# Optimization experiments

Measured on AMD Instinct MI355X. Metric: run time of the kernel, lower is better.

## Reference

```python
import jax, jax.numpy as jnp
import numpy as np

H, W = 64, 64
B, P, F = 8, 512, 512
EXPAND = 0.02      # bbox expansion for soft silhouette (NDC units), DIB-R default
MULT = 1000.0      # DIB-R coordinate multiplier
DELTA = 7000.0     # soft prob falloff in multiplier-scaled squared units, DIB-R default
EPS = 1e-10


def setup_inputs() -> dict:
    key = jax.random.key(0)
    k1, k2, k3 = jax.random.split(key, 3)
    verts = 0.5 * jax.random.normal(k1, (B, P, 3), dtype=jnp.float32)
    faces = jax.random.randint(k2, (B, F, 3), 0, P, dtype=jnp.int32)
    colors = jax.random.uniform(k3, (B, P, 3), dtype=jnp.float32)
    camera_rot = jnp.tile(jnp.eye(3, dtype=jnp.float32)[None], (B, 1, 1))
    camera_pos = jnp.tile(jnp.array([0.0, 0.0, 3.0], dtype=jnp.float32)[None], (B, 1))
    fov_factor = 2.7475  # 1 / tan(fovy/2), fovy ~ 0.7 rad, aspect 1
    camera_proj = jnp.array([[fov_factor], [fov_factor], [-1.0]], dtype=jnp.float32)
    return {"verts": verts, "faces": faces, "camera_rot": camera_rot,
            "camera_pos": camera_pos, "camera_proj": camera_proj, "colors": colors}


def _render_one(verts_p3, faces_f3, rot_33, pos_3, proj_31, colors_p3):
    # --- perspective_projection (pixel2mesh convention: p' = rot^T (p - pos)) ---
    pcam = (verts_p3 - pos_3[None, :]) @ rot_33.T                 # [P,3] camera frame
    xy3 = pcam * proj_31.reshape(3)[None, :]
    xy = xy3[:, :2] / xy3[:, 2:3]                                  # [P,2] NDC
    tri3d = pcam[faces_f3]                                         # [F,3,3]
    tri2d = xy[faces_f3]                                           # [F,3,2]
    normal = jnp.cross(tri3d[:, 1] - tri3d[:, 0], tri3d[:, 2] - tri3d[:, 0])  # [F,3]
    normalz = normal[:, 2]
    normal1 = normal / (jnp.linalg.norm(normal, axis=1, keepdims=True) + 1e-12)
    # per-face vertex colors + hard-mask channel -> [F,3,4] (== color_1xfx12)
    cmask = jnp.ones((faces_f3.shape[0], 3, 1), dtype=colors_p3.dtype)
    cfeat = jnp.concatenate([colors_p3[faces_f3], cmask], axis=2)

    # --- linear_rasterizer: pixel grid in NDC ---
    xs = (2.0 * jnp.arange(W, dtype=jnp.float32) + 1.0 - W) / W
    ys = (H - 2.0 * jnp.arange(H, dtype=jnp.float32) - 1.0) / H
    x0 = xs[None, :, None]                                         # [1,W,1]
    y0 = ys[:, None, None]                                         # [H,1,1]
    ax, ay = tri2d[:, 0, 0], tri2d[:, 0, 1]
    bx, by = tri2d[:, 1, 0], tri2d[:, 1, 1]
    cx, cy = tri2d[:, 2, 0], tri2d[:, 2, 1]
    det = (by - cy) * (ax - cx) + (cx - bx) * (ay - cy)            # [F]
    det_safe = jnp.where(jnp.abs(det) < EPS, EPS, det)
    w0 = ((by - cy) * (x0 - cx) + (cx - bx) * (y0 - cy)) / det_safe  # [H,W,F]
    w1 = ((cy - ay) * (x0 - cx) + (ax - cx) * (y0 - cy)) / det_safe
    w2 = 1.0 - w0 - w1
    z = w0 * tri3d[:, 0, 2] + w1 * tri3d[:, 1, 2] + w2 * tri3d[:, 2, 2]  # [H,W,F]
    covered = (w0 >= 0) & (w1 >= 0) & (w2 >= 0)
    valid = covered & (normalz > 0) & (jnp.abs(det) > EPS)
    # hard z-buffer: camera looks along -z, so nearest face has max z
    zbuf = jnp.where(valid, z, -1e10)
    best = jnp.argmax(zbuf, axis=-1)                               # [H,W]
    anyv = jnp.any(valid, axis=-1)
    gw = lambda w: jnp.take_along_axis(w, best[..., None], axis=-1)[..., 0]
    g0, g1, g2 = gw(w0), gw(w1), gw(w2)
    cb = cfeat[best]                                               # [H,W,3,4]
    feat = (g0[..., None] * cb[..., 0, :] + g1[..., None] * cb[..., 1, :]
            + g2[..., None] * cb[..., 2, :])
    imfeat = jnp.where(anyv[..., None], feat, 0.0)                 # [H,W,4]

    # --- soft silhouette probability ---
    def seg_d2(px, py, qx, qy):
        vx, vy = qx - px, qy - py
        t = jnp.clip(((x0 - px) * vx + (y0 - py) * vy)
                     / (vx * vx + vy * vy + 1e-12), 0.0, 1.0)
        dx, dy = x0 - (px + t * vx), y0 - (py + t * vy)
        return dx * dx + dy * dy
    d2 = jnp.minimum(jnp.minimum(seg_d2(ax, ay, bx, by), seg_d2(bx, by, cx, cy)),
                     seg_d2(cx, cy, ax, ay))
    d2 = jnp.where(covered, 0.0, d2)                               # inside -> 0
    xmin = jnp.minimum(jnp.minimum(ax, bx), cx) - EXPAND
    xmax = jnp.maximum(jnp.maximum(ax, bx), cx) + EXPAND
    ymin = jnp.minimum(jnp.minimum(ay, by), cy) - EXPAND
    ymax = jnp.maximum(jnp.maximum(ay, by), cy) + EXPAND
    in_bbox = (x0 >= xmin) & (x0 <= xmax) & (y0 >= ymin) & (y0 <= ymax)
    contrib = jnp.where(in_bbox, jnp.exp(-d2 * (MULT * MULT) / DELTA), 0.0)
    improb = 1.0 - jnp.prod(1.0 - contrib, axis=-1, keepdims=True)  # [H,W,1]
    return imfeat, improb, normal1


def reference(verts, faces, camera_rot, camera_pos, camera_proj, colors):
    imfeat, improb, normal1 = jax.vmap(_render_one, in_axes=(0, 0, 0, 0, None, 0))(
        verts, faces, camera_rot, camera_pos, camera_proj, colors)
    imrender = imfeat[..., :3]     # [B,H,W,3]
    hardmask = imfeat[..., 3:]     # [B,H,W,1]
    return imrender, improb, normal1, hardmask
```

## Files before the change

kernel.cpp:

```cpp
#include <hip/hip_runtime.h>
#include <math.h>

#define NB 8
#define NP 512
#define NF 512
#define NH 64
#define NW 64
#define FEXPAND 0.02f
#define FEPS 1e-10f

#define IMG_OFF 0
#define PROB_OFF (NB*NH*NW*3)
#define NRM_OFF  (PROB_OFF + NB*NH*NW)
#define MASK_OFF (NRM_OFF + NB*NF*3)

__global__ __launch_bounds__(1024, 8) void render_all(
    const float* __restrict__ verts, const int* __restrict__ faces,
    const float* __restrict__ rot, const float* __restrict__ pos,
    const float* __restrict__ proj, const float* __restrict__ colors,
    float* __restrict__ out)
{
  __shared__ __align__(16) float smem[NF*28];
  __shared__ unsigned short flist[NF];
  __shared__ int wcnt[8];
  __shared__ int Ltot;
  int tid  = threadIdx.x;
  int b    = blockIdx.x >> 6;
  int tile = blockIdx.x & 63;
  int wave = tid >> 6;
  int lane = tid & 63;
  int ix0 = (tile & 7)*8, iy0 = (tile >> 3)*8;
  int ix = ix0 + (lane & 7);
  int iy = iy0 + (lane >> 3);
  float x = (2.0f*ix + 1.0f - 64.0f) * (1.0f/64.0f);
  float y = (64.0f - 2.0f*iy - 1.0f) * (1.0f/64.0f);
  float txlo = (2.0f*ix0 + 1.0f - 64.0f) * (1.0f/64.0f);
  float txhi = (2.0f*(ix0+7) + 1.0f - 64.0f) * (1.0f/64.0f);
  float tyhi = (64.0f - 2.0f*iy0 - 1.0f) * (1.0f/64.0f);
  float tylo = (64.0f - 2.0f*(iy0+7) - 1.0f) * (1.0f/64.0f);

  if (tid < NF) {
    int t = b * NF + tid;
    float p0 = proj[0], p1 = proj[1], p2 = proj[2];
    float R0=rot[b*9+0],R1=rot[b*9+1],R2=rot[b*9+2];
    float R3=rot[b*9+3],R4=rot[b*9+4],R5=rot[b*9+5];
    float R6=rot[b*9+6],R7=rot[b*9+7],R8=rot[b*9+8];
    float ppx=pos[b*3+0], ppy=pos[b*3+1], ppz=pos[b*3+2];
    int idxs[3] = { faces[t*3+0], faces[t*3+1], faces[t*3+2] };
    float X[3],Y[3],Z[3],SX[3],SY[3];
#pragma unroll
    for (int k = 0; k < 3; ++k) {
      const float* v = verts + ((size_t)b*NP + idxs[k])*3;
      float dx = v[0]-ppx, dy = v[1]-ppy, dz = v[2]-ppz;
      float pcx = __fadd_rn(__fadd_rn(__fmul_rn(R0,dx),__fmul_rn(R1,dy)),__fmul_rn(R2,dz));
      float pcy = __fadd_rn(__fadd_rn(__fmul_rn(R3,dx),__fmul_rn(R4,dy)),__fmul_rn(R5,dz));
      float pcz = __fadd_rn(__fadd_rn(__fmul_rn(R6,dx),__fmul_rn(R7,dy)),__fmul_rn(R8,dz));
      X[k]=pcx; Y[k]=pcy; Z[k]=pcz;
      float dn = __fmul_rn(pcz, p2);
      SX[k] = __fdiv_rn(__fmul_rn(pcx, p0), dn);
      SY[k] = __fdiv_rn(__fmul_rn(pcy, p1), dn);
    }
    float e1x=X[1]-X[0], e1y=Y[1]-Y[0], e1z=Z[1]-Z[0];
    float e2x=X[2]-X[0], e2y=Y[2]-Y[0], e2z=Z[2]-Z[0];
    float nzel = __fsub_rn(__fmul_rn(e1x,e2y), __fmul_rn(e1y,e2x));
    if (tile == 0) {
      float m0 = __fmul_rn(e1z, e2y); float nxf = __fmaf_rn(e1y, e2z, -m0);
      float m1 = __fmul_rn(e1x, e2z); float nyf = __fmaf_rn(e1z, e2x, -m1);
      float m2 = __fmul_rn(e1y, e2x); float nzf = __fmaf_rn(e1x, e2y, -m2);
      float nn = __fsqrt_rn(__fadd_rn(__fadd_rn(__fmul_rn(nxf,nxf),__fmul_rn(nyf,nyf)),
                                      __fmul_rn(nzf,nzf)));
      float den = __fadd_rn(nn, 1e-12f);
      out[NRM_OFF + (size_t)t*3+0] = __fdiv_rn(nxf, den);
      out[NRM_OFF + (size_t)t*3+1] = __fdiv_rn(nyf, den);
      out[NRM_OFF + (size_t)t*3+2] = __fdiv_rn(nzf, den);
    }
    float ax=SX[0],ay=SY[0],bx=SX[1],by=SY[1],cx=SX[2],cy=SY[2];
    float det = __fadd_rn(__fmul_rn(__fsub_rn(by,cy),__fsub_rn(ax,cx)),
                          __fmul_rn(__fsub_rn(cx,bx),__fsub_rn(ay,cy)));
    float det_safe = (fabsf(det) < FEPS) ? FEPS : det;
    float validf = ((nzel > 0.0f) && (fabsf(det) > FEPS)) ? 1.0f : 0.0f;
    float* d = &smem[tid*28];
    d[0]=__fsub_rn(by,cy); d[1]=__fsub_rn(cx,bx);
    d[2]=__fsub_rn(cy,ay); d[3]=__fsub_rn(ax,cx);
    d[4]=cx; d[5]=cy; d[6]=det_safe; d[7]=validf;
    d[8]=Z[0]; d[9]=Z[1]; d[10]=Z[2];
    float vx=bx-ax, vy=by-ay;
    d[11]=1.0f/(vx*vx+vy*vy+1e-12f);
    d[20]=vx; d[21]=vy;
    d[12]=fminf(fminf(ax,bx),cx)-FEXPAND; d[13]=fmaxf(fmaxf(ax,bx),cx)+FEXPAND;
    d[14]=fminf(fminf(ay,by),cy)-FEXPAND; d[15]=fmaxf(fmaxf(ay,by),cy)+FEXPAND;
    d[16]=ax; d[17]=ay; d[18]=bx; d[19]=by;
    vx=cx-bx; vy=cy-by;
    d[22]=vx; d[23]=vy; d[26]=1.0f/(vx*vx+vy*vy+1e-12f);
    vx=ax-cx; vy=ay-cy;
    d[24]=vx; d[25]=vy; d[27]=1.0f/(vx*vx+vy*vy+1e-12f);
  }
  __syncthreads();

  bool pass = false;
  if (tid < NF) {
    const float* rr = &smem[tid*28 + 12];
    pass = (rr[1] >= txlo) && (rr[0] <= txhi) && (rr[3] >= tylo) && (rr[2] <= tyhi);
  }
  unsigned long long m = __ballot(pass);
  if (tid < NF && (tid & 63) == 0) wcnt[tid >> 6] = __popcll(m);
  __syncthreads();
  if (tid < NF && pass) {
    int w8 = tid >> 6;
    int off = 0;
#pragma unroll
    for (int i = 0; i < 8; ++i) if (i < w8) off += wcnt[i];
    off += __popcll(m & ((1ull << (tid & 63)) - 1ull));
    flist[off] = (unsigned short)tid;
  }
  if (tid == 0) {
    int s = 0;
#pragma unroll
    for (int i = 0; i < 8; ++i) s += wcnt[i];
    Ltot = s;
  }
  __syncthreads();
  int L = Ltot;

  float bestz = -1e10f;
  int   bestf = 0;
  float bw0 = 0.0f, bw1 = 0.0f, bw2 = 0.0f;
  float prod  = 1.0f;

  int idx = wave;
  int fcur = (idx < L) ? (int)flist[idx] : 0;
  float4 bb = (idx < L) ? *(const float4*)&smem[fcur*28 + 12]
                        : make_float4(0.f,0.f,0.f,0.f);
  while (idx < L) {
    int nidx = idx + 16;
    int fnext = fcur;
    float4 bbn = bb;
    if (nidx < L) {
      fnext = (int)flist[nidx];
      bbn = *(const float4*)&smem[fnext*28 + 12];
    }
    int f = fcur;
    const float* r = &smem[f*28];
    bool inb = (x >= bb.x) && (x <= bb.y) && (y >= bb.z) && (y <= bb.w);
    bool covered = false;
    if (__any(inb)) {
      float4 qe = *(const float4*)(r);
      float4 q1 = *(const float4*)(r + 4);
      float dxc = x - q1.x, dyc = y - q1.y;
      float n0 = __fadd_rn(__fmul_rn(qe.x, dxc), __fmul_rn(qe.y, dyc));
      float n1 = __fadd_rn(__fmul_rn(qe.z, dxc), __fmul_rn(qe.w, dyc));
      bool dsp  = q1.z > 0.0f;
      bool spass = ((n0 == 0.0f) || ((n0 > 0.0f) == dsp)) &&
                   ((n1 == 0.0f) || ((n1 > 0.0f) == dsp));
      bool act = inb && spass;
      if (__any(act)) {
        float4 q2 = *(const float4*)(r + 8);
        float w0 = __fdiv_rn(n0, q1.z);
        float w1 = __fdiv_rn(n1, q1.z);
        float w2 = __fsub_rn(__fsub_rn(1.0f, w0), w1);
        covered = act && (w2 >= 0.0f);
        bool valid = covered && (q1.w > 0.5f);
        float z = __fadd_rn(__fadd_rn(__fmul_rn(w0,q2.x), __fmul_rn(w1,q2.y)),
                            __fmul_rn(w2,q2.z));
        float zval = valid ? z : -1e10f;
        if (zval > bestz) { bestz = zval; bestf = f; bw0 = w0; bw1 = w1; bw2 = w2; }
      }
      if (covered) prod = 0.0f;
      bool needd = inb && !covered && (prod != 0.0f);
      if (__any(needd)) {
        float4 qa = *(const float4*)(r + 16);
        float4 qv = *(const float4*)(r + 20);
        float4 qw = *(const float4*)(r + 24);
        float invAB = r[11];
        float dxa = x - qa.x, dya = y - qa.y;
        float t1 = fminf(fmaxf((dxa*qv.x + dya*qv.y)*invAB, 0.0f), 1.0f);
        float rx = dxa - t1*qv.x, ry = dya - t1*qv.y;
        float d2 = rx*rx + ry*ry;
        float dxb = x - qa.z, dyb = y - qa.w;
        t1 = fminf(fmaxf((dxb*qv.z + dyb*qv.w)*qw.z, 0.0f), 1.0f);
        rx = dxb - t1*qv.z; ry = dyb - t1*qv.w;
        d2 = fminf(d2, rx*rx + ry*ry);
        t1 = fminf(fmaxf((dxc*qw.x + dyc*qw.y)*qw.w, 0.0f), 1.0f);
        rx = dxc - t1*qw.x; ry = dyc - t1*qw.y;
        d2 = fminf(d2, rx*rx + ry*ry);
        if (needd)
          prod *= (1.0f - __expf(d2 * -142.85714285714286f));
      }
    }
    idx = nidx; fcur = fnext; bb = bbn;
  }

  __syncthreads();
  float* comb = smem;
  float* c = comb + (size_t)(wave*64 + lane)*7;
  c[0]=bestz; c[1]=__int_as_float(bestf); c[2]=prod;
  c[3]=bw0; c[4]=bw1; c[5]=bw2;
  __syncthreads();

  if (tid < 64) {
    const float* c0 = comb + (size_t)tid*7;
    float bz = c0[0]; int bf = __float_as_int(c0[1]); float pr = c0[2];
    float w0 = c0[3], w1 = c0[4], w2 = c0[5];
    for (int s = 1; s < 16; ++s) {
      const float* cs = comb + (size_t)(s*64 + tid)*7;
      float oz = cs[0]; int of = __float_as_int(cs[1]);
      if (oz > bz || (oz == bz && of < bf)) { bz = oz; bf = of; w0 = cs[3]; w1 = cs[4]; w2 = cs[5]; }
      pr *= cs[2];
    }
    int av = (bz != -1e10f);
    int t = b * NF + bf;
    const int* fi = faces + (size_t)t*3;
    const float* cb = colors + (size_t)b*NP*3;
    int i0 = fi[0], i1 = fi[1], i2 = fi[2];
    float fr  = w0*cb[i0*3+0] + w1*cb[i1*3+0] + w2*cb[i2*3+0];
    float fgc = w0*cb[i0*3+1] + w1*cb[i1*3+1] + w2*cb[i2*3+1];
    float fb  = w0*cb[i0*3+2] + w1*cb[i1*3+2] + w2*cb[i2*3+2];
    float fa  = __fadd_rn(__fadd_rn(w0, w1), w2);
    int gp = b*4096 + iy*64 + ix;
    out[IMG_OFF + (size_t)gp*3 + 0] = av ? fr  : 0.0f;
    out[IMG_OFF + (size_t)gp*3 + 1] = av ? fgc : 0.0f;
    out[IMG_OFF + (size_t)gp*3 + 2] = av ? fb  : 0.0f;
    out[PROB_OFF + gp] = 1.0f - pr;
    out[MASK_OFF + gp] = av ? fa : 0.0f;
  }
}

extern "C" void kernel_launch(void* const* d_in, const int* in_sizes, int n_in,
                              void* d_out, int out_size, void* d_ws, size_t ws_size,
                              hipStream_t stream) {
  const float* verts  = (const float*)d_in[0];
  const int*   faces  = (const int*)  d_in[1];
  const float* rot    = (const float*)d_in[2];
  const float* pos    = (const float*)d_in[3];
  const float* proj   = (const float*)d_in[4];
  const float* colors = (const float*)d_in[5];
  float* out = (float*)d_out;
  (void)d_ws; (void)ws_size;

  hipLaunchKernelGGL(render_all, dim3(NB*64), dim3(1024), 0, stream,
                     verts, faces, rot, pos, proj, colors, out);
}
```

Baseline: 89.46 us.

## Split renderer into face setup, rasterize, and merge kernels via workspace

Before, every 1024-thread block recomputed all 512 face setups for its batch in shared memory. Now a separate kernel computes per-face records and normals once and writes them to the global workspace. The raster kernel reads those records from global memory, using 4 smaller 256-thread blocks per tile with each wave taking one face slice. A third kernel merges the 16 per-slice partial results. This removes redundant setup work and shared-memory pressure but adds two launches, global round trips of roughly 12.6 MB of partials, and global rather than LDS reads of the face records.

```diff
diff --git a/kernel.cpp b/kernel.cpp
--- a/kernel.cpp
+++ b/kernel.cpp
@@ -14,22 +14,87 @@
 #define NRM_OFF  (PROB_OFF + NB*NH*NW)
 #define MASK_OFF (NRM_OFF + NB*NF*3)
 
-__global__ __launch_bounds__(1024, 8) void render_all(
+#define REC0 4194304
+
+__global__ __launch_bounds__(256, 4) void face_setup(
     const float* __restrict__ verts, const int* __restrict__ faces,
     const float* __restrict__ rot, const float* __restrict__ pos,
-    const float* __restrict__ proj, const float* __restrict__ colors,
+    const float* __restrict__ proj, float* __restrict__ ws,
     float* __restrict__ out)
 {
-  __shared__ __align__(16) float smem[NF*28];
+  int t = blockIdx.x * 256 + threadIdx.x;
+  if (t >= NB * NF) return;
+  int b = t >> 9;
+  float p0 = proj[0], p1 = proj[1], p2 = proj[2];
+  float R0=rot[b*9+0],R1=rot[b*9+1],R2=rot[b*9+2];
+  float R3=rot[b*9+3],R4=rot[b*9+4],R5=rot[b*9+5];
+  float R6=rot[b*9+6],R7=rot[b*9+7],R8=rot[b*9+8];
+  float ppx=pos[b*3+0], ppy=pos[b*3+1], ppz=pos[b*3+2];
+  int idxs[3] = { faces[t*3+0], faces[t*3+1], faces[t*3+2] };
+  float X[3],Y[3],Z[3],SX[3],SY[3];
+#pragma unroll
+  for (int k = 0; k < 3; ++k) {
+    const float* v = verts + ((size_t)b*NP + idxs[k])*3;
+    float dx = v[0]-ppx, dy = v[1]-ppy, dz = v[2]-ppz;
+    float pcx = __fadd_rn(__fadd_rn(__fmul_rn(R0,dx),__fmul_rn(R1,dy)),__fmul_rn(R2,dz));
+    float pcy = __fadd_rn(__fadd_rn(__fmul_rn(R3,dx),__fmul_rn(R4,dy)),__fmul_rn(R5,dz));
+    float pcz = __fadd_rn(__fadd_rn(__fmul_rn(R6,dx),__fmul_rn(R7,dy)),__fmul_rn(R8,dz));
+    X[k]=pcx; Y[k]=pcy; Z[k]=pcz;
+    float dn = __fmul_rn(pcz, p2);
+    SX[k] = __fdiv_rn(__fmul_rn(pcx, p0), dn);
+    SY[k] = __fdiv_rn(__fmul_rn(pcy, p1), dn);
+  }
+  float e1x=X[1]-X[0], e1y=Y[1]-Y[0], e1z=Z[1]-Z[0];
+  float e2x=X[2]-X[0], e2y=Y[2]-Y[0], e2z=Z[2]-Z[0];
+  float nzel = __fsub_rn(__fmul_rn(e1x,e2y), __fmul_rn(e1y,e2x));
+  float m0 = __fmul_rn(e1z, e2y); float nxf = __fmaf_rn(e1y, e2z, -m0);
+  float m1 = __fmul_rn(e1x, e2z); float nyf = __fmaf_rn(e1z, e2x, -m1);
+  float m2 = __fmul_rn(e1y, e2x); float nzf = __fmaf_rn(e1x, e2y, -m2);
+  float nn = __fsqrt_rn(__fadd_rn(__fadd_rn(__fmul_rn(nxf,nxf),__fmul_rn(nyf,nyf)),
+                                  __fmul_rn(nzf,nzf)));
+  float den = __fadd_rn(nn, 1e-12f);
+  out[NRM_OFF + (size_t)t*3+0] = __fdiv_rn(nxf, den);
+  out[NRM_OFF + (size_t)t*3+1] = __fdiv_rn(nyf, den);
+  out[NRM_OFF + (size_t)t*3+2] = __fdiv_rn(nzf, den);
+
+  float ax=SX[0],ay=SY[0],bx=SX[1],by=SY[1],cx=SX[2],cy=SY[2];
+  float det = __fadd_rn(__fmul_rn(__fsub_rn(by,cy),__fsub_rn(ax,cx)),
+                        __fmul_rn(__fsub_rn(cx,bx),__fsub_rn(ay,cy)));
+  float det_safe = (fabsf(det) < FEPS) ? FEPS : det;
+  float validf = ((nzel > 0.0f) && (fabsf(det) > FEPS)) ? 1.0f : 0.0f;
+  float* d = ws + REC0 + (size_t)t*28;
+  d[0]=__fsub_rn(by,cy); d[1]=__fsub_rn(cx,bx);
+  d[2]=__fsub_rn(cy,ay); d[3]=__fsub_rn(ax,cx);
+  d[4]=cx; d[5]=cy; d[6]=det_safe; d[7]=validf;
+  d[8]=Z[0]; d[9]=Z[1]; d[10]=Z[2];
+  float vx=bx-ax, vy=by-ay;
+  d[11]=1.0f/(vx*vx+vy*vy+1e-12f);
+  d[20]=vx; d[21]=vy;
+  d[12]=fminf(fminf(ax,bx),cx)-FEXPAND; d[13]=fmaxf(fmaxf(ax,bx),cx)+FEXPAND;
+  d[14]=fminf(fminf(ay,by),cy)-FEXPAND; d[15]=fmaxf(fmaxf(ay,by),cy)+FEXPAND;
+  d[16]=ax; d[17]=ay; d[18]=bx; d[19]=by;
+  vx=cx-bx; vy=cy-by;
+  d[22]=vx; d[23]=vy; d[26]=1.0f/(vx*vx+vy*vy+1e-12f);
+  vx=ax-cx; vy=ay-cy;
+  d[24]=vx; d[25]=vy; d[27]=1.0f/(vx*vx+vy*vy+1e-12f);
+}
+
+__global__ __launch_bounds__(256, 4) void raster(
+    const float* __restrict__ ws_ro, float* __restrict__ ws,
+    const int* __restrict__ faces)
+{
   __shared__ unsigned short flist[NF];
   __shared__ int wcnt[8];
   __shared__ int Ltot;
   int tid  = threadIdx.x;
-  int b    = blockIdx.x >> 6;
-  int tile = blockIdx.x & 63;
+  int T    = blockIdx.x >> 2;
+  int sb   = blockIdx.x & 3;
   int wave = tid >> 6;
   int lane = tid & 63;
-  int ix0 = (tile & 7)*8, iy0 = (tile >> 3)*8;
+  int slice = sb*4 + wave;
+  int b    = T >> 6;
+  int txy  = T & 63;
+  int ix0 = (txy & 7)*8, iy0 = (txy >> 3)*8;
   int ix = ix0 + (lane & 7);
   int iy = iy0 + (lane >> 3);
   float x = (2.0f*ix + 1.0f - 64.0f) * (1.0f/64.0f);
@@ -38,80 +103,25 @@
   float txhi = (2.0f*(ix0+7) + 1.0f - 64.0f) * (1.0f/64.0f);
   float tyhi = (64.0f - 2.0f*iy0 - 1.0f) * (1.0f/64.0f);
   float tylo = (64.0f - 2.0f*(iy0+7) - 1.0f) * (1.0f/64.0f);
-
-  if (tid < NF) {
-    int t = b * NF + tid;
-    float p0 = proj[0], p1 = proj[1], p2 = proj[2];
-    float R0=rot[b*9+0],R1=rot[b*9+1],R2=rot[b*9+2];
-    float R3=rot[b*9+3],R4=rot[b*9+4],R5=rot[b*9+5];
-    float R6=rot[b*9+6],R7=rot[b*9+7],R8=rot[b*9+8];
-    float ppx=pos[b*3+0], ppy=pos[b*3+1], ppz=pos[b*3+2];
-    int idxs[3] = { faces[t*3+0], faces[t*3+1], faces[t*3+2] };
-    float X[3],Y[3],Z[3],SX[3],SY[3];
-#pragma unroll
-    for (int k = 0; k < 3; ++k) {
-      const float* v = verts + ((size_t)b*NP + idxs[k])*3;
-      float dx = v[0]-ppx, dy = v[1]-ppy, dz = v[2]-ppz;
-      float pcx = __fadd_rn(__fadd_rn(__fmul_rn(R0,dx),__fmul_rn(R1,dy)),__fmul_rn(R2,dz));
-      float pcy = __fadd_rn(__fadd_rn(__fmul_rn(R3,dx),__fmul_rn(R4,dy)),__fmul_rn(R5,dz));
-      float pcz = __fadd_rn(__fadd_rn(__fmul_rn(R6,dx),__fmul_rn(R7,dy)),__fmul_rn(R8,dz));
-      X[k]=pcx; Y[k]=pcy; Z[k]=pcz;
-      float dn = __fmul_rn(pcz, p2);
-      SX[k] = __fdiv_rn(__fmul_rn(pcx, p0), dn);
-      SY[k] = __fdiv_rn(__fmul_rn(pcy, p1), dn);
-    }
-    float e1x=X[1]-X[0], e1y=Y[1]-Y[0], e1z=Z[1]-Z[0];
-    float e2x=X[2]-X[0], e2y=Y[2]-Y[0], e2z=Z[2]-Z[0];
-    float nzel = __fsub_rn(__fmul_rn(e1x,e2y), __fmul_rn(e1y,e2x));
-    if (tile == 0) {
-      float m0 = __fmul_rn(e1z, e2y); float nxf = __fmaf_rn(e1y, e2z, -m0);
-      float m1 = __fmul_rn(e1x, e2z); float nyf = __fmaf_rn(e1z, e2x, -m1);
-      float m2 = __fmul_rn(e1y, e2x); float nzf = __fmaf_rn(e1x, e2y, -m2);
-      float nn = __fsqrt_rn(__fadd_rn(__fadd_rn(__fmul_rn(nxf,nxf),__fmul_rn(nyf,nyf)),
-                                      __fmul_rn(nzf,nzf)));
-      float den = __fadd_rn(nn, 1e-12f);
-      out[NRM_OFF + (size_t)t*3+0] = __fdiv_rn(nxf, den);
-      out[NRM_OFF + (size_t)t*3+1] = __fdiv_rn(nyf, den);
-      out[NRM_OFF + (size_t)t*3+2] = __fdiv_rn(nzf, den);
-    }
-    float ax=SX[0],ay=SY[0],bx=SX[1],by=SY[1],cx=SX[2],cy=SY[2];
-    float det = __fadd_rn(__fmul_rn(__fsub_rn(by,cy),__fsub_rn(ax,cx)),
-                          __fmul_rn(__fsub_rn(cx,bx),__fsub_rn(ay,cy)));
-    float det_safe = (fabsf(det) < FEPS) ? FEPS : det;
-    float validf = ((nzel > 0.0f) && (fabsf(det) > FEPS)) ? 1.0f : 0.0f;
-    float* d = &smem[tid*28];
-    d[0]=__fsub_rn(by,cy); d[1]=__fsub_rn(cx,bx);
-    d[2]=__fsub_rn(cy,ay); d[3]=__fsub_rn(ax,cx);
-    d[4]=cx; d[5]=cy; d[6]=det_safe; d[7]=validf;
-    d[8]=Z[0]; d[9]=Z[1]; d[10]=Z[2];
-    float vx=bx-ax, vy=by-ay;
-    d[11]=1.0f/(vx*vx+vy*vy+1e-12f);
-    d[20]=vx; d[21]=vy;
-    d[12]=fminf(fminf(ax,bx),cx)-FEXPAND; d[13]=fmaxf(fmaxf(ax,bx),cx)+FEXPAND;
-    d[14]=fminf(fminf(ay,by),cy)-FEXPAND; d[15]=fmaxf(fmaxf(ay,by),cy)+FEXPAND;
-    d[16]=ax; d[17]=ay; d[18]=bx; d[19]=by;
-    vx=cx-bx; vy=cy-by;
-    d[22]=vx; d[23]=vy; d[26]=1.0f/(vx*vx+vy*vy+1e-12f);
-    vx=ax-cx; vy=ay-cy;
-    d[24]=vx; d[25]=vy; d[27]=1.0f/(vx*vx+vy*vy+1e-12f);
-  }
-  __syncthreads();
-
-  bool pass = false;
-  if (tid < NF) {
-    const float* rr = &smem[tid*28 + 12];
-    pass = (rr[1] >= txlo) && (rr[0] <= txhi) && (rr[3] >= tylo) && (rr[2] <= tyhi);
-  }
-  unsigned long long m = __ballot(pass);
-  if (tid < NF && (tid & 63) == 0) wcnt[tid >> 6] = __popcll(m);
-  __syncthreads();
-  if (tid < NF && pass) {
-    int w8 = tid >> 6;
-    int off = 0;
-#pragma unroll
-    for (int i = 0; i < 8; ++i) if (i < w8) off += wcnt[i];
-    off += __popcll(m & ((1ull << (tid & 63)) - 1ull));
-    flist[off] = (unsigned short)tid;
+  const float* recs = ws_ro + REC0 + (size_t)b*NF*28;
+
+#pragma unroll
+  for (int r = 0; r < 2; ++r) {
+    int f = r*256 + tid;
+    const float* rr = recs + (size_t)f*28 + 12;
+    bool pass = (rr[1] >= txlo) && (rr[0] <= txhi) && (rr[3] >= tylo) && (rr[2] <= tyhi);
+    unsigned long long m = __ballot(pass);
+    if (lane == 0) wcnt[r*4 + wave] = __popcll(m);
+    __syncthreads();
+    if (pass) {
+      int gi = r*4 + wave;
+      int off = 0;
+#pragma unroll
+      for (int i = 0; i < 8; ++i) if (i < gi) off += wcnt[i];
+      off += __popcll(m & ((1ull << lane) - 1ull));
+      flist[off] = (unsigned short)f;
+    }
+    __syncthreads();
   }
   if (tid == 0) {
     int s = 0;
@@ -127,9 +137,9 @@
   float bw0 = 0.0f, bw1 = 0.0f, bw2 = 0.0f;
   float prod  = 1.0f;
 
-  int idx = wave;
+  int idx = slice;
   int fcur = (idx < L) ? (int)flist[idx] : 0;
-  float4 bb = (idx < L) ? *(const float4*)&smem[fcur*28 + 12]
+  float4 bb = (idx < L) ? *(const float4*)(recs + (size_t)fcur*28 + 12)
                         : make_float4(0.f,0.f,0.f,0.f);
   while (idx < L) {
     int nidx = idx + 16;
@@ -137,10 +147,10 @@
     float4 bbn = bb;
     if (nidx < L) {
       fnext = (int)flist[nidx];
-      bbn = *(const float4*)&smem[fnext*28 + 12];
+      bbn = *(const float4*)(recs + (size_t)fnext*28 + 12);
     }
     int f = fcur;
-    const float* r = &smem[f*28];
+    const float* r = recs + (size_t)f*28;
     bool inb = (x >= bb.x) && (x <= bb.y) && (y >= bb.z) && (y <= bb.w);
     bool covered = false;
     if (__any(inb)) {
@@ -190,39 +200,53 @@
     idx = nidx; fcur = fnext; bb = bbn;
   }
 
-  __syncthreads();
-  float* comb = smem;
-  float* c = comb + (size_t)(wave*64 + lane)*7;
-  c[0]=bestz; c[1]=__int_as_float(bestf); c[2]=prod;
-  c[3]=bw0; c[4]=bw1; c[5]=bw2;
-  __syncthreads();
-
-  if (tid < 64) {
-    const float* c0 = comb + (size_t)tid*7;
-    float bz = c0[0]; int bf = __float_as_int(c0[1]); float pr = c0[2];
-    float w0 = c0[3], w1 = c0[4], w2 = c0[5];
-    for (int s = 1; s < 16; ++s) {
-      const float* cs = comb + (size_t)(s*64 + tid)*7;
-      float oz = cs[0]; int of = __float_as_int(cs[1]);
-      if (oz > bz || (oz == bz && of < bf)) { bz = oz; bf = of; w0 = cs[3]; w1 = cs[4]; w2 = cs[5]; }
-      pr *= cs[2];
-    }
-    int av = (bz != -1e10f);
-    int t = b * NF + bf;
-    const int* fi = faces + (size_t)t*3;
-    const float* cb = colors + (size_t)b*NP*3;
-    int i0 = fi[0], i1 = fi[1], i2 = fi[2];
-    float fr  = w0*cb[i0*3+0] + w1*cb[i1*3+0] + w2*cb[i2*3+0];
-    float fgc = w0*cb[i0*3+1] + w1*cb[i1*3+1] + w2*cb[i2*3+1];
-    float fb  = w0*cb[i0*3+2] + w1*cb[i1*3+2] + w2*cb[i2*3+2];
-    float fa  = __fadd_rn(__fadd_rn(w0, w1), w2);
-    int gp = b*4096 + iy*64 + ix;
-    out[IMG_OFF + (size_t)gp*3 + 0] = av ? fr  : 0.0f;
-    out[IMG_OFF + (size_t)gp*3 + 1] = av ? fgc : 0.0f;
-    out[IMG_OFF + (size_t)gp*3 + 2] = av ? fb  : 0.0f;
-    out[PROB_OFF + gp] = 1.0f - pr;
-    out[MASK_OFF + gp] = av ? fa : 0.0f;
-  }
+  size_t base = ((size_t)T*16 + slice)*64 + lane;
+  ws[ (size_t)0*512*16*64 + base] = bestz;
+  ws[ (size_t)1*512*16*64 + base] = __int_as_float(bestf);
+  ws[ (size_t)2*512*16*64 + base] = prod;
+  ws[ (size_t)3*512*16*64 + base] = bw0;
+  ws[ (size_t)4*512*16*64 + base] = bw1;
+  ws[ (size_t)5*512*16*64 + base] = bw2;
+}
+
+__global__ __launch_bounds__(256, 4) void merge(
+    const float* __restrict__ ws, const int* __restrict__ faces,
+    const float* __restrict__ colors, float* __restrict__ out)
+{
+  int gp = blockIdx.x * 256 + threadIdx.x;
+  int b  = gp >> 12;
+  int p  = gp & 4095;
+  int iy = p >> 6, ix = p & 63;
+  int T  = b*64 + (iy >> 3)*8 + (ix >> 3);
+  int lane = (iy & 7)*8 + (ix & 7);
+  const size_t C = (size_t)512*16*64;
+  size_t base = ((size_t)T*16)*64 + lane;
+
+  float bz = ws[0*C + base]; int bf = __float_as_int(ws[1*C + base]);
+  float pr = ws[2*C + base];
+  float w0 = ws[3*C + base], w1 = ws[4*C + base], w2 = ws[5*C + base];
+  for (int s = 1; s < 16; ++s) {
+    size_t o = base + (size_t)s*64;
+    float oz = ws[0*C + o]; int of = __float_as_int(ws[1*C + o]);
+    if (oz > bz || (oz == bz && of < bf)) {
+      bz = oz; bf = of; w0 = ws[3*C + o]; w1 = ws[4*C + o]; w2 = ws[5*C + o];
+    }
+    pr *= ws[2*C + o];
+  }
+  int av = (bz != -1e10f);
+  int t = b * NF + bf;
+  const int* fi = faces + (size_t)t*3;
+  const float* cb = colors + (size_t)b*NP*3;
+  int i0 = fi[0], i1 = fi[1], i2 = fi[2];
+  float fr  = w0*cb[i0*3+0] + w1*cb[i1*3+0] + w2*cb[i2*3+0];
+  float fgc = w0*cb[i0*3+1] + w1*cb[i1*3+1] + w2*cb[i2*3+1];
+  float fb  = w0*cb[i0*3+2] + w1*cb[i1*3+2] + w2*cb[i2*3+2];
+  float fa  = __fadd_rn(__fadd_rn(w0, w1), w2);
+  out[IMG_OFF + (size_t)gp*3 + 0] = av ? fr  : 0.0f;
+  out[IMG_OFF + (size_t)gp*3 + 1] = av ? fgc : 0.0f;
+  out[IMG_OFF + (size_t)gp*3 + 2] = av ? fb  : 0.0f;
+  out[PROB_OFF + gp] = 1.0f - pr;
+  out[MASK_OFF + gp] = av ? fa : 0.0f;
 }
 
 extern "C" void kernel_launch(void* const* d_in, const int* in_sizes, int n_in,
@@ -235,8 +259,12 @@
   const float* proj   = (const float*)d_in[4];
   const float* colors = (const float*)d_in[5];
   float* out = (float*)d_out;
-  (void)d_ws; (void)ws_size;
-
-  hipLaunchKernelGGL(render_all, dim3(NB*64), dim3(1024), 0, stream,
-                     verts, faces, rot, pos, proj, colors, out);
-}
+  float* ws  = (float*)d_ws;
+
+  hipLaunchKernelGGL(face_setup, dim3((NB*NF)/256), dim3(256), 0, stream,
+                     verts, faces, rot, pos, proj, ws, out);
+  hipLaunchKernelGGL(raster, dim3(512*4), dim3(256), 0, stream,
+                     ws, ws, faces);
+  hipLaunchKernelGGL(merge, dim3((NB*NH*NW)/256), dim3(256), 0, stream,
+                     ws, faces, colors, out);
+}
```

Measured after the change: 118.2 us. 1.32x slower.

## Shrink per-face LDS records and parallelize vertex projection across all threads

Applied to the files above, without the earlier changes.

Face setup now projects each face-vertex in parallel across all 1024 threads through a scratch LDS buffer, instead of 512 threads each doing three vertices serially. The per-face record shrinks from 28 to 16 floats. Edge vectors, vertex positions and inverse squared edge lengths for the soft distance term are rebuilt from the stored edge coefficients inside the hot loop. This trades extra ALU work, including three reciprocals per face in the distance path, for a cheaper prologue and fewer LDS reads. Reconstructing the vertices from differences may change float rounding slightly.

```diff
diff --git a/kernel.cpp b/kernel.cpp
--- a/kernel.cpp
+++ b/kernel.cpp
@@ -20,7 +20,8 @@
     const float* __restrict__ proj, const float* __restrict__ colors,
     float* __restrict__ out)
 {
-  __shared__ __align__(16) float smem[NF*28];
+  __shared__ __align__(16) float recs[NF*16];
+  __shared__ float scratch[NF*15];
   __shared__ unsigned short flist[NF];
   __shared__ int wcnt[8];
   __shared__ int Ltot;
@@ -39,31 +40,39 @@
   float tyhi = (64.0f - 2.0f*iy0 - 1.0f) * (1.0f/64.0f);
   float tylo = (64.0f - 2.0f*(iy0+7) - 1.0f) * (1.0f/64.0f);
 
-  if (tid < NF) {
-    int t = b * NF + tid;
+  {
     float p0 = proj[0], p1 = proj[1], p2 = proj[2];
     float R0=rot[b*9+0],R1=rot[b*9+1],R2=rot[b*9+2];
     float R3=rot[b*9+3],R4=rot[b*9+4],R5=rot[b*9+5];
     float R6=rot[b*9+6],R7=rot[b*9+7],R8=rot[b*9+8];
     float ppx=pos[b*3+0], ppy=pos[b*3+1], ppz=pos[b*3+2];
-    int idxs[3] = { faces[t*3+0], faces[t*3+1], faces[t*3+2] };
-    float X[3],Y[3],Z[3],SX[3],SY[3];
-#pragma unroll
-    for (int k = 0; k < 3; ++k) {
-      const float* v = verts + ((size_t)b*NP + idxs[k])*3;
+    for (int i = tid; i < 3*NF; i += 1024) {
+      int k = i >> 9, f = i & 511;
+      int vi = faces[((size_t)(b*NF + f))*3 + k];
+      const float* v = verts + ((size_t)b*NP + vi)*3;
       float dx = v[0]-ppx, dy = v[1]-ppy, dz = v[2]-ppz;
       float pcx = __fadd_rn(__fadd_rn(__fmul_rn(R0,dx),__fmul_rn(R1,dy)),__fmul_rn(R2,dz));
       float pcy = __fadd_rn(__fadd_rn(__fmul_rn(R3,dx),__fmul_rn(R4,dy)),__fmul_rn(R5,dz));
       float pcz = __fadd_rn(__fadd_rn(__fmul_rn(R6,dx),__fmul_rn(R7,dy)),__fmul_rn(R8,dz));
-      X[k]=pcx; Y[k]=pcy; Z[k]=pcz;
       float dn = __fmul_rn(pcz, p2);
-      SX[k] = __fdiv_rn(__fmul_rn(pcx, p0), dn);
-      SY[k] = __fdiv_rn(__fmul_rn(pcy, p1), dn);
-    }
-    float e1x=X[1]-X[0], e1y=Y[1]-Y[0], e1z=Z[1]-Z[0];
-    float e2x=X[2]-X[0], e2y=Y[2]-Y[0], e2z=Z[2]-Z[0];
+      float sx = __fdiv_rn(__fmul_rn(pcx, p0), dn);
+      float sy = __fdiv_rn(__fmul_rn(pcy, p1), dn);
+      float* s = &scratch[f*15 + k*5];
+      s[0]=pcx; s[1]=pcy; s[2]=pcz; s[3]=sx; s[4]=sy;
+    }
+  }
+  __syncthreads();
+
+  if (tid < NF) {
+    const float* s = &scratch[tid*15];
+    float X0=s[0], Y0=s[1], Z0=s[2], ax=s[3], ay=s[4];
+    float X1=s[5], Y1=s[6], Z1=s[7], bx=s[8], by=s[9];
+    float X2=s[10],Y2=s[11],Z2=s[12],cx=s[13],cy=s[14];
+    float e1x=X1-X0, e1y=Y1-Y0, e1z=Z1-Z0;
+    float e2x=X2-X0, e2y=Y2-Y0, e2z=Z2-Z0;
     float nzel = __fsub_rn(__fmul_rn(e1x,e2y), __fmul_rn(e1y,e2x));
     if (tile == 0) {
+      int t = b * NF + tid;
       float m0 = __fmul_rn(e1z, e2y); float nxf = __fmaf_rn(e1y, e2z, -m0);
       float m1 = __fmul_rn(e1x, e2z); float nyf = __fmaf_rn(e1z, e2x, -m1);
       float m2 = __fmul_rn(e1y, e2x); float nzf = __fmaf_rn(e1x, e2y, -m2);
@@ -74,32 +83,23 @@
       out[NRM_OFF + (size_t)t*3+1] = __fdiv_rn(nyf, den);
       out[NRM_OFF + (size_t)t*3+2] = __fdiv_rn(nzf, den);
     }
-    float ax=SX[0],ay=SY[0],bx=SX[1],by=SY[1],cx=SX[2],cy=SY[2];
     float det = __fadd_rn(__fmul_rn(__fsub_rn(by,cy),__fsub_rn(ax,cx)),
                           __fmul_rn(__fsub_rn(cx,bx),__fsub_rn(ay,cy)));
     float det_safe = (fabsf(det) < FEPS) ? FEPS : det;
     float validf = ((nzel > 0.0f) && (fabsf(det) > FEPS)) ? 1.0f : 0.0f;
-    float* d = &smem[tid*28];
+    float* d = &recs[tid*16];
     d[0]=__fsub_rn(by,cy); d[1]=__fsub_rn(cx,bx);
     d[2]=__fsub_rn(cy,ay); d[3]=__fsub_rn(ax,cx);
     d[4]=cx; d[5]=cy; d[6]=det_safe; d[7]=validf;
-    d[8]=Z[0]; d[9]=Z[1]; d[10]=Z[2];
-    float vx=bx-ax, vy=by-ay;
-    d[11]=1.0f/(vx*vx+vy*vy+1e-12f);
-    d[20]=vx; d[21]=vy;
+    d[8]=Z0; d[9]=Z1; d[10]=Z2; d[11]=0.0f;
     d[12]=fminf(fminf(ax,bx),cx)-FEXPAND; d[13]=fmaxf(fmaxf(ax,bx),cx)+FEXPAND;
     d[14]=fminf(fminf(ay,by),cy)-FEXPAND; d[15]=fmaxf(fmaxf(ay,by),cy)+FEXPAND;
-    d[16]=ax; d[17]=ay; d[18]=bx; d[19]=by;
-    vx=cx-bx; vy=cy-by;
-    d[22]=vx; d[23]=vy; d[26]=1.0f/(vx*vx+vy*vy+1e-12f);
-    vx=ax-cx; vy=ay-cy;
-    d[24]=vx; d[25]=vy; d[27]=1.0f/(vx*vx+vy*vy+1e-12f);
   }
   __syncthreads();
 
   bool pass = false;
   if (tid < NF) {
-    const float* rr = &smem[tid*28 + 12];
+    const float* rr = &recs[tid*16 + 12];
     pass = (rr[1] >= txlo) && (rr[0] <= txhi) && (rr[3] >= tylo) && (rr[2] <= tyhi);
   }
   unsigned long long m = __ballot(pass);
@@ -129,7 +129,7 @@
 
   int idx = wave;
   int fcur = (idx < L) ? (int)flist[idx] : 0;
-  float4 bb = (idx < L) ? *(const float4*)&smem[fcur*28 + 12]
+  float4 bb = (idx < L) ? *(const float4*)&recs[fcur*16 + 12]
                         : make_float4(0.f,0.f,0.f,0.f);
   while (idx < L) {
     int nidx = idx + 16;
@@ -137,15 +137,15 @@
     float4 bbn = bb;
     if (nidx < L) {
       fnext = (int)flist[nidx];
-      bbn = *(const float4*)&smem[fnext*28 + 12];
+      bbn = *(const float4*)&recs[fnext*16 + 12];
     }
     int f = fcur;
-    const float* r = &smem[f*28];
     bool inb = (x >= bb.x) && (x <= bb.y) && (y >= bb.z) && (y <= bb.w);
     bool covered = false;
     if (__any(inb)) {
-      float4 qe = *(const float4*)(r);
-      float4 q1 = *(const float4*)(r + 4);
+      const float* h = &recs[f*16];
+      float4 qe = *(const float4*)(h);
+      float4 q1 = *(const float4*)(h + 4);
       float dxc = x - q1.x, dyc = y - q1.y;
       float n0 = __fadd_rn(__fmul_rn(qe.x, dxc), __fmul_rn(qe.y, dyc));
       float n1 = __fadd_rn(__fmul_rn(qe.z, dxc), __fmul_rn(qe.w, dyc));
@@ -154,7 +154,7 @@
                    ((n1 == 0.0f) || ((n1 > 0.0f) == dsp));
       bool act = inb && spass;
       if (__any(act)) {
-        float4 q2 = *(const float4*)(r + 8);
+        float4 q2 = *(const float4*)(h + 8);
         float w0 = __fdiv_rn(n0, q1.z);
         float w1 = __fdiv_rn(n1, q1.z);
         float w2 = __fsub_rn(__fsub_rn(1.0f, w0), w1);
@@ -168,20 +168,24 @@
       if (covered) prod = 0.0f;
       bool needd = inb && !covered && (prod != 0.0f);
       if (__any(needd)) {
-        float4 qa = *(const float4*)(r + 16);
-        float4 qv = *(const float4*)(r + 20);
-        float4 qw = *(const float4*)(r + 24);
-        float invAB = r[11];
-        float dxa = x - qa.x, dya = y - qa.y;
-        float t1 = fminf(fmaxf((dxa*qv.x + dya*qv.y)*invAB, 0.0f), 1.0f);
-        float rx = dxa - t1*qv.x, ry = dya - t1*qv.y;
+        float axd = q1.x + qe.w, ayd = q1.y - qe.z;
+        float bxd = q1.x - qe.y, byd = q1.y + qe.x;
+        float vABx = -qe.y - qe.w, vABy = qe.x + qe.z;
+        float vBCx = qe.y, vBCy = -qe.x;
+        float vCAx = qe.w, vCAy = -qe.z;
+        float invAB = 1.0f/(vABx*vABx + vABy*vABy + 1e-12f);
+        float invBC = 1.0f/(vBCx*vBCx + vBCy*vBCy + 1e-12f);
+        float invCA = 1.0f/(vCAx*vCAx + vCAy*vCAy + 1e-12f);
+        float dxa = x - axd, dya = y - ayd;
+        float t1 = fminf(fmaxf((dxa*vABx + dya*vABy)*invAB, 0.0f), 1.0f);
+        float rx = dxa - t1*vABx, ry = dya - t1*vABy;
         float d2 = rx*rx + ry*ry;
-        float dxb = x - qa.z, dyb = y - qa.w;
-        t1 = fminf(fmaxf((dxb*qv.z + dyb*qv.w)*qw.z, 0.0f), 1.0f);
-        rx = dxb - t1*qv.z; ry = dyb - t1*qv.w;
+        float dxb = x - bxd, dyb = y - byd;
+        t1 = fminf(fmaxf((dxb*vBCx + dyb*vBCy)*invBC, 0.0f), 1.0f);
+        rx = dxb - t1*vBCx; ry = dyb - t1*vBCy;
         d2 = fminf(d2, rx*rx + ry*ry);
-        t1 = fminf(fmaxf((dxc*qw.x + dyc*qw.y)*qw.w, 0.0f), 1.0f);
-        rx = dxc - t1*qw.x; ry = dyc - t1*qw.y;
+        t1 = fminf(fmaxf((dxc*vCAx + dyc*vCAy)*invCA, 0.0f), 1.0f);
+        rx = dxc - t1*vCAx; ry = dyc - t1*vCAy;
         d2 = fminf(d2, rx*rx + ry*ry);
         if (needd)
           prod *= (1.0f - __expf(d2 * -142.85714285714286f));
@@ -191,7 +195,7 @@
   }
 
   __syncthreads();
-  float* comb = smem;
+  float* comb = recs;
   float* c = comb + (size_t)(wave*64 + lane)*7;
   c[0]=bestz; c[1]=__int_as_float(bestf); c[2]=prod;
   c[3]=bw0; c[4]=bw1; c[5]=bw2;
```

New measurement: 98.44 us. 10.0% more time.
